# Optimization experiments

Measured on AMD Instinct MI355X. Metric: run time of the kernel, lower is better.

Reference implementation:

```python
import jax, jax.numpy as jnp
import numpy as np

N_NODES = 100000
N_EDGES = 1600000
N_GRAPHS = 1000
HID = 64
NEG_SLOPE = 0.2


def _glorot(key, shape):
    fan_in, fan_out = shape[0], shape[-1]
    lim = float(np.sqrt(6.0 / (fan_in + fan_out)))
    return jax.random.uniform(key, shape, jnp.float32, -lim, lim)


def setup_inputs() -> dict:
    key = jax.random.key(0)
    ks = jax.random.split(key, 20)
    x = jax.random.normal(ks[0], (N_NODES, 1), jnp.float32)
    edge_index = jax.random.randint(ks[1], (2, N_EDGES), 0, N_NODES, jnp.int64)
    batch = jnp.sort(jax.random.randint(ks[2], (N_NODES,), 0, N_GRAPHS, jnp.int64))
    inp = {"x": x, "edge_index": edge_index, "batch": batch}
    # GATv2Conv layer 1 (in=3 -> out=HID, 1 head)
    inp["Wl1"] = _glorot(ks[3], (3, HID)); inp["bl1"] = jnp.zeros((HID,), jnp.float32)
    inp["Wr1"] = _glorot(ks[4], (3, HID)); inp["br1"] = jnp.zeros((HID,), jnp.float32)
    inp["a1"] = _glorot(ks[5], (HID, 1))[:, 0]; inp["b1"] = jnp.zeros((HID,), jnp.float32)
    # GATv2Conv layer 2 (HID -> HID)
    inp["Wl2"] = _glorot(ks[6], (HID, HID)); inp["bl2"] = jnp.zeros((HID,), jnp.float32)
    inp["Wr2"] = _glorot(ks[7], (HID, HID)); inp["br2"] = jnp.zeros((HID,), jnp.float32)
    inp["a2"] = _glorot(ks[8], (HID, 1))[:, 0]; inp["b2"] = jnp.zeros((HID,), jnp.float32)
    # lin2 (HID -> 2)
    inp["W3"] = _glorot(ks[9], (HID, 2)); inp["b3"] = jnp.zeros((2,), jnp.float32)
    return inp


def gatv2_layer(x, src, dst, Wl, bl, Wr, br, a, b):
    """GATv2Conv, 1 head, add_self_loops=True, negative_slope=0.2."""
    n = x.shape[0]
    xl = x @ Wl + bl  # source-side transform [N, C]
    xr = x @ Wr + br  # target-side transform [N, C]
    loops = jnp.arange(n, dtype=src.dtype)
    s = jnp.concatenate([src, loops])
    d = jnp.concatenate([dst, loops])
    # per-edge attention logit: a^T LeakyReLU(xl[j] + xr[i])
    e = jax.nn.leaky_relu(xl[s] + xr[d], NEG_SLOPE) @ a  # [E+N]
    # segment softmax over incoming edges of each dst node
    m = jax.ops.segment_max(e, d, num_segments=n)
    ex = jnp.exp(e - m[d])
    denom = jax.ops.segment_sum(ex, d, num_segments=n)
    alpha = ex / denom[d]
    out = jax.ops.segment_sum(alpha[:, None] * xl[s], d, num_segments=n)
    return out + b


def reference(x, edge_index, batch, Wl1, bl1, Wr1, br1, a1, b1,
              Wl2, bl2, Wr2, br2, a2, b2, W3, b3):
    n = x.shape[0]
    src, dst = edge_index[0], edge_index[1]
    ones = jnp.ones((src.shape[0],), jnp.float32)
    deg_in = jax.ops.segment_sum(ones, dst, num_segments=n)   # bincount(dst)
    deg_out = jax.ops.segment_sum(ones, src, num_segments=n)  # bincount(src)
    h = jnp.concatenate([x, deg_in[:, None], deg_out[:, None]], axis=1)  # [N,3]
    h = gatv2_layer(h, src, dst, Wl1, bl1, Wr1, br1, a1, b1)
    h = jnp.tanh(h)
    h = gatv2_layer(h, src, dst, Wl2, bl2, Wr2, br2, a2, b2)
    # global_max_pool over graphs
    g = jax.ops.segment_max(h, batch, num_segments=N_GRAPHS)  # [G, HID]
    return g @ W3 + b3  # [G, 2]
```

## Files before the change

kernel.cpp:

```cpp
#include <hip/hip_runtime.h>
#include <hip/hip_bf16.h>
#include <hip/hip_fp16.h>

#define HID 64
#define NEG_SLOPE 0.2f
#define BLK_E 8192
#define EDGE_CAP 6144


__global__ void k_hist2(const int* __restrict__ src, const int* __restrict__ dst,
                        int* __restrict__ histS, int* __restrict__ histD,
                        int E, int NB, int NBLK) {
    __shared__ int hs[512], hd[512];
    int t = threadIdx.x, blk = blockIdx.x;
    for (int b = t; b < NB; b += 1024) { hs[b] = 0; hd[b] = 0; }
    __syncthreads();
    int base = blk * BLK_E;
    #pragma unroll
    for (int k = 0; k < BLK_E / 1024; ++k) {
        int i = base + k * 1024 + t;
        if (i < E) {
            atomicAdd(&hs[src[i] >> 8], 1);
            atomicAdd(&hd[dst[i] >> 8], 1);
        }
    }
    __syncthreads();
    for (int b = t; b < NB; b += 1024) {
        histS[b * NBLK + blk] = hs[b];
        histD[b * NBLK + blk] = hd[b];
    }
}

__global__ void k_binscan(int* __restrict__ histS, int* __restrict__ histD,
                          int* __restrict__ totS, int* __restrict__ totD,
                          int NB, int NBLK) {
    __shared__ int s[256];
    int b = blockIdx.x;
    int* hist = histS; int* tot = totS;
    if (b >= NB) { b -= NB; hist = histD; tot = totD; }
    int t = threadIdx.x;
    int v = (t < NBLK) ? hist[b * NBLK + t] : 0;
    s[t] = v;
    __syncthreads();
    for (int o = 1; o < 256; o <<= 1) {
        int u = (t >= o) ? s[t - o] : 0;
        __syncthreads();
        s[t] += u;
        __syncthreads();
    }
    if (t < NBLK) hist[b * NBLK + t] = s[t] - v;
    if (t == 255) tot[b] = s[255];
}

__global__ void k_binoffset(const int* __restrict__ totS, const int* __restrict__ totD,
                            int* __restrict__ bsS, int* __restrict__ bsD,
                            int NB, int E, int* __restrict__ row_off, int N) {
    __shared__ int s[512];
    int t = threadIdx.x;
    int v = (t < NB) ? totS[t] : 0;
    s[t] = v; __syncthreads();
    for (int o = 1; o < 512; o <<= 1) {
        int u = (t >= o) ? s[t - o] : 0;
        __syncthreads(); s[t] += u; __syncthreads();
    }
    if (t < NB) bsS[t] = s[t] - v;
    if (t == 0) bsS[NB] = E;
    __syncthreads();
    v = (t < NB) ? totD[t] : 0;
    s[t] = v; __syncthreads();
    for (int o = 1; o < 512; o <<= 1) {
        int u = (t >= o) ? s[t - o] : 0;
        __syncthreads(); s[t] += u; __syncthreads();
    }
    if (t < NB) bsD[t] = s[t] - v;
    if (t == 0) { bsD[NB] = E; row_off[N] = E; }
}

__global__ void k_scatter_bins(const int* __restrict__ src, const int* __restrict__ dst,
                               const int* __restrict__ histS, const int* __restrict__ histD,
                               const int* __restrict__ bsS, const int* __restrict__ bsD,
                               unsigned* __restrict__ packS, unsigned* __restrict__ packD,
                               int E, int NB, int NBLK) {
    __shared__ int baseS[512], baseD[512];
    int t = threadIdx.x, blk = blockIdx.x;
    for (int b = t; b < NB; b += 1024) {
        baseS[b] = bsS[b] + histS[b * NBLK + blk];
        baseD[b] = bsD[b] + histD[b * NBLK + blk];
    }
    __syncthreads();
    int base = blk * BLK_E;
    #pragma unroll
    for (int k = 0; k < BLK_E / 1024; ++k) {
        int i = base + k * 1024 + t;
        if (i < E) {
            int sv = src[i], dv = dst[i];
            int pD = atomicAdd(&baseD[dv >> 8], 1);
            packD[pD] = ((unsigned)(dv & 255) << 24) | (unsigned)sv;
            int pS = atomicAdd(&baseS[sv >> 8], 1);
            packS[pS] = (unsigned)(sv & 255);
        }
    }
}

__global__ void k_csr_bin(const unsigned* __restrict__ packD, const int* __restrict__ bsD,
                          int* __restrict__ row_off, float* __restrict__ deg_in,
                          int* __restrict__ csr_src, int N) {
    __shared__ int cnt[256], off[256], cur[256];
    __shared__ unsigned eb[EDGE_CAP];
    int b = blockIdx.x, t = threadIdx.x;
    int lo = bsD[b], hi = bsD[b + 1], ne = hi - lo;
    bool fits = (ne <= EDGE_CAP);
    if (t < 256) cnt[t] = 0;
    __syncthreads();
    for (int i = t; i < ne; i += 1024) {
        unsigned v = packD[lo + i];
        if (fits) eb[i] = v;
        atomicAdd(&cnt[v >> 24], 1);
    }
    __syncthreads();
    if (t < 256) off[t] = cnt[t];
    __syncthreads();
    for (int o = 1; o < 256; o <<= 1) {
        int u = 0;
        if (t < 256 && t >= o) u = off[t - o];
        __syncthreads();
        if (t < 256) off[t] += u;
        __syncthreads();
    }
    if (t < 256) {
        int ex = off[t] - cnt[t];
        cur[t] = lo + ex;
        int node = b * 256 + t;
        if (node < N) {
            row_off[node] = lo + ex;
            deg_in[node] = (float)cnt[t];
        }
    }
    __syncthreads();
    for (int i = t; i < ne; i += 1024) {
        unsigned v = fits ? eb[i] : packD[lo + i];
        int pos = atomicAdd(&cur[v >> 24], 1);
        csr_src[pos] = (int)(v & 0xFFFFFFu);
    }
}

__global__ void k_cnt_bin(const unsigned* __restrict__ packS, const int* __restrict__ bsS,
                          float* __restrict__ deg_out, int N) {
    __shared__ int cnt[256];
    int b = blockIdx.x, t = threadIdx.x;
    int lo = bsS[b], hi = bsS[b + 1];
    if (t < 256) cnt[t] = 0;
    __syncthreads();
    for (int i = lo + t; i < hi; i += 1024) atomicAdd(&cnt[packS[i] & 255], 1);
    __syncthreads();
    if (t < 256) {
        int node = b * 256 + t;
        if (node < N) deg_out[node] = (float)cnt[t];
    }
}


__device__ __forceinline__ float4 h4f(uint2 r) {
    __half2 p0 = __builtin_bit_cast(__half2, r.x);
    __half2 p1 = __builtin_bit_cast(__half2, r.y);
    float2 q0 = __half22float2(p0);
    float2 q1 = __half22float2(p1);
    return make_float4(q0.x, q0.y, q1.x, q1.y);
}

__global__ void k_xfrm1(const float* __restrict__ x, const float* __restrict__ deg_in,
                        const float* __restrict__ deg_out,
                        const float* __restrict__ Wl, const float* __restrict__ bl,
                        const float* __restrict__ Wr, const float* __restrict__ br,
                        __half* __restrict__ A, __half* __restrict__ B, int N) {
    int idx = blockIdx.x * blockDim.x + threadIdx.x;
    if (idx >= N * HID) return;
    int n = idx >> 6, c = idx & 63;
    float h0 = x[n], h1 = deg_in[n], h2 = deg_out[n];
    A[idx] = __float2half(h0 * Wl[c] + h1 * Wl[HID + c] + h2 * Wl[2 * HID + c] + bl[c]);
    B[idx] = __float2half(h0 * Wr[c] + h1 * Wr[HID + c] + h2 * Wr[2 * HID + c] + br[c]);
}

template <bool TANH>
__global__ void k_gat_fused(const int* __restrict__ csr_src, const int* __restrict__ row_off,
                            const __half* __restrict__ Ah, const __half* __restrict__ Bh,
                            const float* __restrict__ aw, const float* __restrict__ bias,
                            float* __restrict__ out, int N) {
    int tid = blockIdx.x * blockDim.x + threadIdx.x;
    int d = tid >> 4;
    int gl = threadIdx.x & 15;
    if (d >= N) return;

    const uint2* A2 = (const uint2*)Ah;
    const uint2* B2 = (const uint2*)Bh;
    float4 awv = ((const float4*)aw)[gl];
    float4 xr = h4f(B2[(size_t)d * 16 + gl]);

    float4 as = h4f(A2[(size_t)d * 16 + gl]);
    float4 v;
    v.x = as.x + xr.x; v.x = fmaxf(v.x, NEG_SLOPE * v.x);
    v.y = as.y + xr.y; v.y = fmaxf(v.y, NEG_SLOPE * v.y);
    v.z = as.z + xr.z; v.z = fmaxf(v.z, NEG_SLOPE * v.z);
    v.w = as.w + xr.w; v.w = fmaxf(v.w, NEG_SLOPE * v.w);
    float t = fmaf(v.x, awv.x, fmaf(v.y, awv.y, fmaf(v.z, awv.z, v.w * awv.w)));
    #pragma unroll
    for (int o = 1; o < 16; o <<= 1) t += __shfl_xor(t, o);
    float m = t;
    float denom = 1.0f;
    float4 acc = as;

    int lo = row_off[d], hi = row_off[d + 1];
    int k = lo;
    for (; k + 1 < hi; k += 2) {
        int s0 = csr_src[k], s1 = csr_src[k + 1];
        float4 a0 = h4f(A2[(size_t)s0 * 16 + gl]);
        float4 a1 = h4f(A2[(size_t)s1 * 16 + gl]);
        float4 v0, v1;
        v0.x = a0.x + xr.x; v0.x = fmaxf(v0.x, NEG_SLOPE * v0.x);
        v0.y = a0.y + xr.y; v0.y = fmaxf(v0.y, NEG_SLOPE * v0.y);
        v0.z = a0.z + xr.z; v0.z = fmaxf(v0.z, NEG_SLOPE * v0.z);
        v0.w = a0.w + xr.w; v0.w = fmaxf(v0.w, NEG_SLOPE * v0.w);
        v1.x = a1.x + xr.x; v1.x = fmaxf(v1.x, NEG_SLOPE * v1.x);
        v1.y = a1.y + xr.y; v1.y = fmaxf(v1.y, NEG_SLOPE * v1.y);
        v1.z = a1.z + xr.z; v1.z = fmaxf(v1.z, NEG_SLOPE * v1.z);
        v1.w = a1.w + xr.w; v1.w = fmaxf(v1.w, NEG_SLOPE * v1.w);
        float t0 = fmaf(v0.x, awv.x, fmaf(v0.y, awv.y, fmaf(v0.z, awv.z, v0.w * awv.w)));
        float t1 = fmaf(v1.x, awv.x, fmaf(v1.y, awv.y, fmaf(v1.z, awv.z, v1.w * awv.w)));
        #pragma unroll
        for (int o = 1; o < 16; o <<= 1) { t0 += __shfl_xor(t0, o); t1 += __shfl_xor(t1, o); }
        if (t0 > m) {
            float sc = __expf(m - t0);
            acc.x *= sc; acc.y *= sc; acc.z *= sc; acc.w *= sc;
            denom *= sc; m = t0;
        }
        float w0 = __expf(t0 - m);
        denom += w0;
        acc.x = fmaf(w0, a0.x, acc.x); acc.y = fmaf(w0, a0.y, acc.y);
        acc.z = fmaf(w0, a0.z, acc.z); acc.w = fmaf(w0, a0.w, acc.w);
        if (t1 > m) {
            float sc = __expf(m - t1);
            acc.x *= sc; acc.y *= sc; acc.z *= sc; acc.w *= sc;
            denom *= sc; m = t1;
        }
        float w1 = __expf(t1 - m);
        denom += w1;
        acc.x = fmaf(w1, a1.x, acc.x); acc.y = fmaf(w1, a1.y, acc.y);
        acc.z = fmaf(w1, a1.z, acc.z); acc.w = fmaf(w1, a1.w, acc.w);
    }
    if (k < hi) {
        int s0 = csr_src[k];
        float4 a0 = h4f(A2[(size_t)s0 * 16 + gl]);
        float4 v0;
        v0.x = a0.x + xr.x; v0.x = fmaxf(v0.x, NEG_SLOPE * v0.x);
        v0.y = a0.y + xr.y; v0.y = fmaxf(v0.y, NEG_SLOPE * v0.y);
        v0.z = a0.z + xr.z; v0.z = fmaxf(v0.z, NEG_SLOPE * v0.z);
        v0.w = a0.w + xr.w; v0.w = fmaxf(v0.w, NEG_SLOPE * v0.w);
        float t0 = fmaf(v0.x, awv.x, fmaf(v0.y, awv.y, fmaf(v0.z, awv.z, v0.w * awv.w)));
        #pragma unroll
        for (int o = 1; o < 16; o <<= 1) t0 += __shfl_xor(t0, o);
        if (t0 > m) {
            float sc = __expf(m - t0);
            acc.x *= sc; acc.y *= sc; acc.z *= sc; acc.w *= sc;
            denom *= sc; m = t0;
        }
        float w0 = __expf(t0 - m);
        denom += w0;
        acc.x = fmaf(w0, a0.x, acc.x); acc.y = fmaf(w0, a0.y, acc.y);
        acc.z = fmaf(w0, a0.z, acc.z); acc.w = fmaf(w0, a0.w, acc.w);
    }

    float4 bv = ((const float4*)bias)[gl];
    float inv = 1.0f / denom;
    float4 o4;
    o4.x = acc.x * inv + bv.x;
    o4.y = acc.y * inv + bv.y;
    o4.z = acc.z * inv + bv.z;
    o4.w = acc.w * inv + bv.w;
    if (TANH) {
        o4.x = tanhf(o4.x); o4.y = tanhf(o4.y); o4.z = tanhf(o4.z); o4.w = tanhf(o4.w);
    }
    ((float4*)out)[(size_t)d * 16 + gl] = o4;
}

__global__ __launch_bounds__(512) void k_xfrm2(
        const float* __restrict__ H,
        const float* __restrict__ Wl, const float* __restrict__ bl,
        const float* __restrict__ Wr, const float* __restrict__ br,
        __half* __restrict__ A, __half* __restrict__ B, int N) {
    __shared__ float wls[4096];
    __shared__ float wrs[4096];
    __shared__ float hst[64 * 66];
    int t = threadIdx.x;
    int base = blockIdx.x * 64;

    ((float4*)wls)[t * 2]     = ((const float4*)Wl)[t * 2];
    ((float4*)wls)[t * 2 + 1] = ((const float4*)Wl)[t * 2 + 1];
    ((float4*)wrs)[t * 2]     = ((const float4*)Wr)[t * 2];
    ((float4*)wrs)[t * 2 + 1] = ((const float4*)Wr)[t * 2 + 1];

    #pragma unroll
    for (int u = 0; u < 2; ++u) {
        int j = t * 2 + u;
        int nd = j >> 4, c4 = j & 15;
        int node = base + nd;
        float4 hv = (node < N) ? ((const float4*)H)[(size_t)node * 16 + c4]
                               : make_float4(0.f, 0.f, 0.f, 0.f);
        hst[(c4 * 4 + 0) * 66 + nd] = hv.x;
        hst[(c4 * 4 + 1) * 66 + nd] = hv.y;
        hst[(c4 * 4 + 2) * 66 + nd] = hv.z;
        hst[(c4 * 4 + 3) * 66 + nd] = hv.w;
    }
    __syncthreads();

    int w = t >> 6, l = t & 63;
    float acL[8] = {0, 0, 0, 0, 0, 0, 0, 0};
    float acR[8] = {0, 0, 0, 0, 0, 0, 0, 0};
    #pragma unroll 4
    for (int kk = 0; kk < 64; ++kk) {
        float hv = hst[kk * 66 + l];
        const float4* wl4 = (const float4*)&wls[kk * 64 + w * 8];
        const float4* wr4 = (const float4*)&wrs[kk * 64 + w * 8];
        float4 w0 = wl4[0], w1 = wl4[1];
        float4 r0 = wr4[0], r1 = wr4[1];
        acL[0] = fmaf(hv, w0.x, acL[0]); acL[1] = fmaf(hv, w0.y, acL[1]);
        acL[2] = fmaf(hv, w0.z, acL[2]); acL[3] = fmaf(hv, w0.w, acL[3]);
        acL[4] = fmaf(hv, w1.x, acL[4]); acL[5] = fmaf(hv, w1.y, acL[5]);
        acL[6] = fmaf(hv, w1.z, acL[6]); acL[7] = fmaf(hv, w1.w, acL[7]);
        acR[0] = fmaf(hv, r0.x, acR[0]); acR[1] = fmaf(hv, r0.y, acR[1]);
        acR[2] = fmaf(hv, r0.z, acR[2]); acR[3] = fmaf(hv, r0.w, acR[3]);
        acR[4] = fmaf(hv, r1.x, acR[4]); acR[5] = fmaf(hv, r1.y, acR[5]);
        acR[6] = fmaf(hv, r1.z, acR[6]); acR[7] = fmaf(hv, r1.w, acR[7]);
    }

    int node = base + l;
    if (node < N) {
        float4 bl0 = ((const float4*)bl)[w * 2], bl1 = ((const float4*)bl)[w * 2 + 1];
        float4 br0 = ((const float4*)br)[w * 2], br1 = ((const float4*)br)[w * 2 + 1];
        __half2* A2 = (__half2*)A;
        __half2* B2 = (__half2*)B;
        size_t bo = (size_t)node * 32 + w * 4;
        A2[bo + 0] = __floats2half2_rn(acL[0] + bl0.x, acL[1] + bl0.y);
        A2[bo + 1] = __floats2half2_rn(acL[2] + bl0.z, acL[3] + bl0.w);
        A2[bo + 2] = __floats2half2_rn(acL[4] + bl1.x, acL[5] + bl1.y);
        A2[bo + 3] = __floats2half2_rn(acL[6] + bl1.z, acL[7] + bl1.w);
        B2[bo + 0] = __floats2half2_rn(acR[0] + br0.x, acR[1] + br0.y);
        B2[bo + 1] = __floats2half2_rn(acR[2] + br0.z, acR[3] + br0.w);
        B2[bo + 2] = __floats2half2_rn(acR[4] + br1.x, acR[5] + br1.y);
        B2[bo + 3] = __floats2half2_rn(acR[6] + br1.z, acR[7] + br1.w);
    }
}

__global__ void k_gbounds(const int* __restrict__ batch, int* __restrict__ gstart,
                          int* __restrict__ gend, int N) {
    int i = blockIdx.x * blockDim.x + threadIdx.x;
    if (i >= N) return;
    int g = batch[i];
    if (i == 0 || batch[i - 1] != g) gstart[g] = i;
    if (i == N - 1 || batch[i + 1] != g) gend[g] = i + 1;
}

__global__ void k_pool_seg(const float* __restrict__ C, const float* __restrict__ b2,
                           const int* __restrict__ gstart, const int* __restrict__ gend,
                           float* __restrict__ gout, int G) {
    int w = (int)((blockIdx.x * (size_t)blockDim.x + threadIdx.x) >> 6);
    int lane = threadIdx.x & 63;
    if (w >= G) return;
    float acc = -INFINITY;
    int lo = gstart[w], hi = gend[w];
    for (int i = lo; i < hi; ++i) acc = fmaxf(acc, C[(size_t)i * HID + lane]);
    gout[(size_t)w * HID + lane] = acc + b2[lane];
}

__global__ void k_final(const float* __restrict__ gout, const float* __restrict__ W3,
                        const float* __restrict__ b3, float* __restrict__ out, int G) {
    int idx = blockIdx.x * blockDim.x + threadIdx.x;
    if (idx >= G * 2) return;
    int gi = idx >> 1, j = idx & 1;
    float sum = b3[j];
    #pragma unroll 8
    for (int kk = 0; kk < HID; ++kk) sum += gout[(size_t)gi * HID + kk] * W3[kk * 2 + j];
    out[idx] = sum;
}

extern "C" void kernel_launch(void* const* d_in, const int* in_sizes, int n_in,
                              void* d_out, int out_size, void* d_ws, size_t ws_size,
                              hipStream_t stream) {
    const float* x     = (const float*)d_in[0];
    const int*   ei    = (const int*)d_in[1];
    const int*   batch = (const int*)d_in[2];
    const float* Wl1 = (const float*)d_in[3];
    const float* bl1 = (const float*)d_in[4];
    const float* Wr1 = (const float*)d_in[5];
    const float* br1 = (const float*)d_in[6];
    const float* a1  = (const float*)d_in[7];
    const float* b1  = (const float*)d_in[8];
    const float* Wl2 = (const float*)d_in[9];
    const float* bl2 = (const float*)d_in[10];
    const float* Wr2 = (const float*)d_in[11];
    const float* br2 = (const float*)d_in[12];
    const float* a2  = (const float*)d_in[13];
    const float* b2  = (const float*)d_in[14];
    const float* W3  = (const float*)d_in[15];
    const float* b3  = (const float*)d_in[16];

    const int N = in_sizes[0];
    const int E = in_sizes[1] / 2;
    const int G = out_size / 2;
    const int NB = (N + 255) >> 8;
    const int NBLK = (E + BLK_E - 1) / BLK_E;

    float* ws = (float*)d_ws;
    size_t off = 0;
    float*  C  = ws + off; off += (size_t)N * HID;
    __half* Ah = (__half*)(ws + off); off += (size_t)N * HID / 2;
    __half* Bh = (__half*)(ws + off); off += (size_t)N * HID / 2;
    int*   row_off = (int*)(ws + off); off += N + 1;
    int*   csr_src = (int*)(ws + off); off += E;
    float* deg_in  = ws + off; off += N;
    float* deg_out = ws + off; off += N;
    int*   bsS  = (int*)(ws + off); off += NB + 1;
    int*   bsD  = (int*)(ws + off); off += NB + 1;
    int*   totS = (int*)(ws + off); off += NB;
    int*   totD = (int*)(ws + off); off += NB;
    int*   gstart = (int*)(ws + off); off += G;
    int*   gend   = (int*)(ws + off); off += G;
    float* gout   = ws + off; off += (size_t)G * HID;

    unsigned* packD = (unsigned*)C;
    unsigned* packS = packD + E;
    int* histS = (int*)(packS + E);
    int* histD = histS + (size_t)NB * NBLK;

    const int* src  = ei;
    const int* dstp = ei + E;

    const int BT = 256;
    dim3 blk(BT);
    int grid_nodeC = (N * HID + BT - 1) / BT;
    int grid_g16   = (int)(((size_t)N * 16 + BT - 1) / BT);
    int grid_x2    = (N + 63) / 64;

    k_hist2<<<NBLK, 1024, 0, stream>>>(src, dstp, histS, histD, E, NB, NBLK);
    k_binscan<<<2 * NB, 256, 0, stream>>>(histS, histD, totS, totD, NB, NBLK);
    k_binoffset<<<1, 512, 0, stream>>>(totS, totD, bsS, bsD, NB, E, row_off, N);
    k_scatter_bins<<<NBLK, 1024, 0, stream>>>(src, dstp, histS, histD, bsS, bsD,
                                              packS, packD, E, NB, NBLK);
    k_csr_bin<<<NB, 1024, 0, stream>>>(packD, bsD, row_off, deg_in, csr_src, N);
    k_cnt_bin<<<NB, 1024, 0, stream>>>(packS, bsS, deg_out, N);

    hipMemsetAsync(gstart, 0, 2 * (size_t)G * sizeof(int), stream);
    k_gbounds<<<(N + BT - 1) / BT, blk, 0, stream>>>(batch, gstart, gend, N);

    k_xfrm1<<<grid_nodeC, blk, 0, stream>>>(x, deg_in, deg_out, Wl1, bl1, Wr1, br1, Ah, Bh, N);
    k_gat_fused<true><<<grid_g16, blk, 0, stream>>>(csr_src, row_off, Ah, Bh, a1, b1, C, N);

    k_xfrm2<<<grid_x2, 512, 0, stream>>>(C, Wl2, bl2, Wr2, br2, Ah, Bh, N);
    k_gat_fused<false><<<grid_g16, blk, 0, stream>>>(csr_src, row_off, Ah, Bh, a2, b2, C, N);

    k_pool_seg<<<(G * 64 + BT - 1) / BT, blk, 0, stream>>>(C, b2, gstart, gend, gout, G);
    k_final<<<(G * 2 + BT - 1) / BT, blk, 0, stream>>>(gout, W3, b3, (float*)d_out, G);
}
```

Baseline: 247.2 us.

## Sort GAT nodes by in-degree and use 4 lanes per node with packed fp16 math

Adds a counting-sort pass (histogram, scan, scatter) that orders destination nodes by in-degree, so neighbouring lanes in a wavefront walk edge lists of similar length and divergence is reduced. The fused GAT kernel now gives each node 4 lanes handling 16 channels each, with 32-byte row loads, instead of 16 lanes with 4 channels each. This cuts shuffle reductions and raises per-lane memory-level parallelism. The attention logit's add and LeakyReLU are done in packed fp16, which can change numerics slightly. Online-softmax rescaling is merged into one check per edge pair, and three small extra kernels are added to build the permutation.

```diff
diff --git a/kernel.cpp b/kernel.cpp
--- a/kernel.cpp
+++ b/kernel.cpp
@@ -6,6 +6,9 @@
 #define NEG_SLOPE 0.2f
 #define BLK_E 8192
 #define EDGE_CAP 6144
+#define NDB 16
+
+typedef _Float16 f16x2 __attribute__((ext_vector_type(2)));
 
 
 __global__ void k_hist2(const int* __restrict__ src, const int* __restrict__ dst,
@@ -160,13 +163,48 @@
 }
 
 
-__device__ __forceinline__ float4 h4f(uint2 r) {
-    __half2 p0 = __builtin_bit_cast(__half2, r.x);
-    __half2 p1 = __builtin_bit_cast(__half2, r.y);
-    float2 q0 = __half22float2(p0);
-    float2 q1 = __half22float2(p1);
-    return make_float4(q0.x, q0.y, q1.x, q1.y);
-}
+__global__ void k_deghist(const float* __restrict__ deg_in, int* __restrict__ dhist, int N) {
+    __shared__ int h[64];
+    int t = threadIdx.x, b = blockIdx.x;
+    if (t < 64) h[t] = 0;
+    __syncthreads();
+    int chunk = (N + NDB - 1) / NDB;
+    int lo = b * chunk, hi = lo + chunk; if (hi > N) hi = N;
+    for (int i = lo + t; i < hi; i += 1024) {
+        int dg = (int)deg_in[i]; if (dg > 63) dg = 63;
+        atomicAdd(&h[dg], 1);
+    }
+    __syncthreads();
+    if (t < 64) dhist[t * NDB + b] = h[t];
+}
+
+__global__ void k_degscan(int* __restrict__ dhist) {
+    __shared__ int s[1024];
+    int t = threadIdx.x;
+    int v = dhist[t];
+    s[t] = v; __syncthreads();
+    for (int o = 1; o < 1024; o <<= 1) {
+        int u = (t >= o) ? s[t - o] : 0;
+        __syncthreads(); s[t] += u; __syncthreads();
+    }
+    dhist[t] = s[t] - v;
+}
+
+__global__ void k_degscatter(const float* __restrict__ deg_in, const int* __restrict__ dhist,
+                             int* __restrict__ perm, int N) {
+    __shared__ int cur[64];
+    int t = threadIdx.x, b = blockIdx.x;
+    if (t < 64) cur[t] = dhist[t * NDB + b];
+    __syncthreads();
+    int chunk = (N + NDB - 1) / NDB;
+    int lo = b * chunk, hi = lo + chunk; if (hi > N) hi = N;
+    for (int i = lo + t; i < hi; i += 1024) {
+        int dg = (int)deg_in[i]; if (dg > 63) dg = 63;
+        int p = atomicAdd(&cur[dg], 1);
+        perm[p] = i;
+    }
+}
+
 
 __global__ void k_xfrm1(const float* __restrict__ x, const float* __restrict__ deg_in,
                         const float* __restrict__ deg_out,
@@ -181,105 +219,136 @@
     B[idx] = __float2half(h0 * Wr[c] + h1 * Wr[HID + c] + h2 * Wr[2 * HID + c] + br[c]);
 }
 
+struct H8 { f16x2 h[8]; };
+
+__device__ __forceinline__ f16x2 bch2(unsigned u) {
+    return __builtin_bit_cast(f16x2, u);
+}
+
+__device__ __forceinline__ H8 ldrow(const uint4* __restrict__ T, size_t base) {
+    uint4 r0 = T[base], r1 = T[base + 1];
+    H8 o;
+    o.h[0] = bch2(r0.x); o.h[1] = bch2(r0.y); o.h[2] = bch2(r0.z); o.h[3] = bch2(r0.w);
+    o.h[4] = bch2(r1.x); o.h[5] = bch2(r1.y); o.h[6] = bch2(r1.z); o.h[7] = bch2(r1.w);
+    return o;
+}
+
+__device__ __forceinline__ float logit16(const H8& a, const H8& x,
+                                         const float* __restrict__ awf, f16x2 ns2) {
+    float t = 0.0f;
+    #pragma unroll
+    for (int j = 0; j < 8; ++j) {
+        f16x2 s = a.h[j] + x.h[j];
+        f16x2 l = __builtin_elementwise_max(s, ns2 * s);
+        t = fmaf((float)l.x, awf[2 * j], t);
+        t = fmaf((float)l.y, awf[2 * j + 1], t);
+    }
+    return t;
+}
+
+__device__ __forceinline__ void accum16(float* __restrict__ acc, const H8& a, float w) {
+    #pragma unroll
+    for (int j = 0; j < 8; ++j) {
+        acc[2 * j]     = fmaf((float)a.h[j].x, w, acc[2 * j]);
+        acc[2 * j + 1] = fmaf((float)a.h[j].y, w, acc[2 * j + 1]);
+    }
+}
+
 template <bool TANH>
 __global__ void k_gat_fused(const int* __restrict__ csr_src, const int* __restrict__ row_off,
+                            const int* __restrict__ perm,
                             const __half* __restrict__ Ah, const __half* __restrict__ Bh,
                             const float* __restrict__ aw, const float* __restrict__ bias,
                             float* __restrict__ out, int N) {
     int tid = blockIdx.x * blockDim.x + threadIdx.x;
-    int d = tid >> 4;
-    int gl = threadIdx.x & 15;
-    if (d >= N) return;
-
-    const uint2* A2 = (const uint2*)Ah;
-    const uint2* B2 = (const uint2*)Bh;
-    float4 awv = ((const float4*)aw)[gl];
-    float4 xr = h4f(B2[(size_t)d * 16 + gl]);
-
-    float4 as = h4f(A2[(size_t)d * 16 + gl]);
-    float4 v;
-    v.x = as.x + xr.x; v.x = fmaxf(v.x, NEG_SLOPE * v.x);
-    v.y = as.y + xr.y; v.y = fmaxf(v.y, NEG_SLOPE * v.y);
-    v.z = as.z + xr.z; v.z = fmaxf(v.z, NEG_SLOPE * v.z);
-    v.w = as.w + xr.w; v.w = fmaxf(v.w, NEG_SLOPE * v.w);
-    float t = fmaf(v.x, awv.x, fmaf(v.y, awv.y, fmaf(v.z, awv.z, v.w * awv.w)));
-    #pragma unroll
-    for (int o = 1; o < 16; o <<= 1) t += __shfl_xor(t, o);
-    float m = t;
-    float denom = 1.0f;
-    float4 acc = as;
+    int r = tid >> 2;
+    int gl = threadIdx.x & 3;
+    if (r >= N) return;
+    int d = perm[r];
+
+    const uint4* A16 = (const uint4*)Ah;
+    const uint4* B16 = (const uint4*)Bh;
+    f16x2 ns2;
+    ns2.x = (_Float16)NEG_SLOPE; ns2.y = (_Float16)NEG_SLOPE;
+
+    float awf[16];
+    {
+        const float4* a4 = (const float4*)aw;
+        #pragma unroll
+        for (int j = 0; j < 4; ++j) {
+            float4 v = a4[gl * 4 + j];
+            awf[4 * j] = v.x; awf[4 * j + 1] = v.y; awf[4 * j + 2] = v.z; awf[4 * j + 3] = v.w;
+        }
+    }
+
+    size_t rowbase = (size_t)d * 8 + gl * 2;
+    H8 xh = ldrow(B16, rowbase);
+    H8 as = ldrow(A16, rowbase);
+
+    float t = logit16(as, xh, awf, ns2);
+    t += __shfl_xor(t, 1); t += __shfl_xor(t, 2);
+    float m = t, denom = 1.0f;
+    float acc[16];
+    #pragma unroll
+    for (int j = 0; j < 8; ++j) {
+        acc[2 * j] = (float)as.h[j].x;
+        acc[2 * j + 1] = (float)as.h[j].y;
+    }
 
     int lo = row_off[d], hi = row_off[d + 1];
     int k = lo;
     for (; k + 1 < hi; k += 2) {
         int s0 = csr_src[k], s1 = csr_src[k + 1];
-        float4 a0 = h4f(A2[(size_t)s0 * 16 + gl]);
-        float4 a1 = h4f(A2[(size_t)s1 * 16 + gl]);
-        float4 v0, v1;
-        v0.x = a0.x + xr.x; v0.x = fmaxf(v0.x, NEG_SLOPE * v0.x);
-        v0.y = a0.y + xr.y; v0.y = fmaxf(v0.y, NEG_SLOPE * v0.y);
-        v0.z = a0.z + xr.z; v0.z = fmaxf(v0.z, NEG_SLOPE * v0.z);
-        v0.w = a0.w + xr.w; v0.w = fmaxf(v0.w, NEG_SLOPE * v0.w);
-        v1.x = a1.x + xr.x; v1.x = fmaxf(v1.x, NEG_SLOPE * v1.x);
-        v1.y = a1.y + xr.y; v1.y = fmaxf(v1.y, NEG_SLOPE * v1.y);
-        v1.z = a1.z + xr.z; v1.z = fmaxf(v1.z, NEG_SLOPE * v1.z);
-        v1.w = a1.w + xr.w; v1.w = fmaxf(v1.w, NEG_SLOPE * v1.w);
-        float t0 = fmaf(v0.x, awv.x, fmaf(v0.y, awv.y, fmaf(v0.z, awv.z, v0.w * awv.w)));
-        float t1 = fmaf(v1.x, awv.x, fmaf(v1.y, awv.y, fmaf(v1.z, awv.z, v1.w * awv.w)));
-        #pragma unroll
-        for (int o = 1; o < 16; o <<= 1) { t0 += __shfl_xor(t0, o); t1 += __shfl_xor(t1, o); }
+        H8 a0 = ldrow(A16, (size_t)s0 * 8 + gl * 2);
+        H8 a1 = ldrow(A16, (size_t)s1 * 8 + gl * 2);
+        float t0 = logit16(a0, xh, awf, ns2);
+        float t1 = logit16(a1, xh, awf, ns2);
+        t0 += __shfl_xor(t0, 1); t1 += __shfl_xor(t1, 1);
+        t0 += __shfl_xor(t0, 2); t1 += __shfl_xor(t1, 2);
+        float mx = fmaxf(t0, t1);
+        if (mx > m) {
+            float sc = __expf(m - mx);
+            denom *= sc;
+            #pragma unroll
+            for (int j = 0; j < 16; ++j) acc[j] *= sc;
+            m = mx;
+        }
+        float w0 = __expf(t0 - m), w1 = __expf(t1 - m);
+        denom += w0 + w1;
+        accum16(acc, a0, w0);
+        accum16(acc, a1, w1);
+    }
+    if (k < hi) {
+        int s0 = csr_src[k];
+        H8 a0 = ldrow(A16, (size_t)s0 * 8 + gl * 2);
+        float t0 = logit16(a0, xh, awf, ns2);
+        t0 += __shfl_xor(t0, 1); t0 += __shfl_xor(t0, 2);
         if (t0 > m) {
             float sc = __expf(m - t0);
-            acc.x *= sc; acc.y *= sc; acc.z *= sc; acc.w *= sc;
-            denom *= sc; m = t0;
+            denom *= sc;
+            #pragma unroll
+            for (int j = 0; j < 16; ++j) acc[j] *= sc;
+            m = t0;
         }
         float w0 = __expf(t0 - m);
         denom += w0;
-        acc.x = fmaf(w0, a0.x, acc.x); acc.y = fmaf(w0, a0.y, acc.y);
-        acc.z = fmaf(w0, a0.z, acc.z); acc.w = fmaf(w0, a0.w, acc.w);
-        if (t1 > m) {
-            float sc = __expf(m - t1);
-            acc.x *= sc; acc.y *= sc; acc.z *= sc; acc.w *= sc;
-            denom *= sc; m = t1;
-        }
-        float w1 = __expf(t1 - m);
-        denom += w1;
-        acc.x = fmaf(w1, a1.x, acc.x); acc.y = fmaf(w1, a1.y, acc.y);
-        acc.z = fmaf(w1, a1.z, acc.z); acc.w = fmaf(w1, a1.w, acc.w);
-    }
-    if (k < hi) {
-        int s0 = csr_src[k];
-        float4 a0 = h4f(A2[(size_t)s0 * 16 + gl]);
-        float4 v0;
-        v0.x = a0.x + xr.x; v0.x = fmaxf(v0.x, NEG_SLOPE * v0.x);
-        v0.y = a0.y + xr.y; v0.y = fmaxf(v0.y, NEG_SLOPE * v0.y);
-        v0.z = a0.z + xr.z; v0.z = fmaxf(v0.z, NEG_SLOPE * v0.z);
-        v0.w = a0.w + xr.w; v0.w = fmaxf(v0.w, NEG_SLOPE * v0.w);
-        float t0 = fmaf(v0.x, awv.x, fmaf(v0.y, awv.y, fmaf(v0.z, awv.z, v0.w * awv.w)));
-        #pragma unroll
-        for (int o = 1; o < 16; o <<= 1) t0 += __shfl_xor(t0, o);
-        if (t0 > m) {
-            float sc = __expf(m - t0);
-            acc.x *= sc; acc.y *= sc; acc.z *= sc; acc.w *= sc;
-            denom *= sc; m = t0;
-        }
-        float w0 = __expf(t0 - m);
-        denom += w0;
-        acc.x = fmaf(w0, a0.x, acc.x); acc.y = fmaf(w0, a0.y, acc.y);
-        acc.z = fmaf(w0, a0.z, acc.z); acc.w = fmaf(w0, a0.w, acc.w);
-    }
-
-    float4 bv = ((const float4*)bias)[gl];
+        accum16(acc, a0, w0);
+    }
+
     float inv = 1.0f / denom;
-    float4 o4;
-    o4.x = acc.x * inv + bv.x;
-    o4.y = acc.y * inv + bv.y;
-    o4.z = acc.z * inv + bv.z;
-    o4.w = acc.w * inv + bv.w;
-    if (TANH) {
-        o4.x = tanhf(o4.x); o4.y = tanhf(o4.y); o4.z = tanhf(o4.z); o4.w = tanhf(o4.w);
-    }
-    ((float4*)out)[(size_t)d * 16 + gl] = o4;
+    const float4* b4 = (const float4*)bias;
+    float4* o4 = (float4*)out;
+    #pragma unroll
+    for (int j = 0; j < 4; ++j) {
+        float4 bv = b4[gl * 4 + j];
+        float4 o;
+        o.x = acc[4 * j] * inv + bv.x;
+        o.y = acc[4 * j + 1] * inv + bv.y;
+        o.z = acc[4 * j + 2] * inv + bv.z;
+        o.w = acc[4 * j + 3] * inv + bv.w;
+        if (TANH) { o.x = tanhf(o.x); o.y = tanhf(o.y); o.z = tanhf(o.z); o.w = tanhf(o.w); }
+        o4[(size_t)d * 16 + gl * 4 + j] = o;
+    }
 }
 
 __global__ __launch_bounds__(512) void k_xfrm2(
@@ -418,6 +487,8 @@
     int*   csr_src = (int*)(ws + off); off += E;
     float* deg_in  = ws + off; off += N;
     float* deg_out = ws + off; off += N;
+    int*   perm    = (int*)(ws + off); off += N;
+    int*   dhist   = (int*)(ws + off); off += 1024;
     int*   bsS  = (int*)(ws + off); off += NB + 1;
     int*   bsD  = (int*)(ws + off); off += NB + 1;
     int*   totS = (int*)(ws + off); off += NB;
@@ -437,7 +508,7 @@
     const int BT = 256;
     dim3 blk(BT);
     int grid_nodeC = (N * HID + BT - 1) / BT;
-    int grid_g16   = (int)(((size_t)N * 16 + BT - 1) / BT);
+    int grid_g4    = (int)(((size_t)N * 4 + BT - 1) / BT);
     int grid_x2    = (N + 63) / 64;
 
     k_hist2<<<NBLK, 1024, 0, stream>>>(src, dstp, histS, histD, E, NB, NBLK);
@@ -448,14 +519,18 @@
     k_csr_bin<<<NB, 1024, 0, stream>>>(packD, bsD, row_off, deg_in, csr_src, N);
     k_cnt_bin<<<NB, 1024, 0, stream>>>(packS, bsS, deg_out, N);
 
-    hipMemsetAsync(gstart, 0, 2 * (size_t)G * sizeof(int), stream);
+    k_deghist<<<NDB, 1024, 0, stream>>>(deg_in, dhist, N);
+    k_degscan<<<1, 1024, 0, stream>>>(dhist);
+    k_degscatter<<<NDB, 1024, 0, stream>>>(deg_in, dhist, perm, N);
+
+    (void)hipMemsetAsync(gstart, 0, 2 * (size_t)G * sizeof(int), stream);
     k_gbounds<<<(N + BT - 1) / BT, blk, 0, stream>>>(batch, gstart, gend, N);
 
     k_xfrm1<<<grid_nodeC, blk, 0, stream>>>(x, deg_in, deg_out, Wl1, bl1, Wr1, br1, Ah, Bh, N);
-    k_gat_fused<true><<<grid_g16, blk, 0, stream>>>(csr_src, row_off, Ah, Bh, a1, b1, C, N);
+    k_gat_fused<true><<<grid_g4, blk, 0, stream>>>(csr_src, row_off, perm, Ah, Bh, a1, b1, C, N);
 
     k_xfrm2<<<grid_x2, 512, 0, stream>>>(C, Wl2, bl2, Wr2, br2, Ah, Bh, N);
-    k_gat_fused<false><<<grid_g16, blk, 0, stream>>>(csr_src, row_off, Ah, Bh, a2, b2, C, N);
+    k_gat_fused<false><<<grid_g4, blk, 0, stream>>>(csr_src, row_off, perm, Ah, Bh, a2, b2, C, N);
 
     k_pool_seg<<<(G * 64 + BT - 1) / BT, blk, 0, stream>>>(C, b2, gstart, gend, gout, G);
     k_final<<<(G * 2 + BT - 1) / BT, blk, 0, stream>>>(gout, W3, b3, (float*)d_out, G);
```

Measured after the change: 246.0 us. No clear change (-0.5%).
